# Performance work log

Hardware: AMD Instinct MI355X
Metric: run time of the kernel (lower is better)

Reference implementation:

```python
import math
import jax, jax.numpy as jnp
import numpy as np

NUM_EMBED = 2048
EMBED_FEATS = 64
IN_FEATS = 512
B, T = 16, 4096
COMMITMENT_COST = 0.25


def setup_inputs() -> dict:
    key = jax.random.key(0)
    k1, k2, k3, k4 = jax.random.split(key, 4)
    x = jax.random.normal(k1, (B, IN_FEATS, T), dtype=jnp.float32)
    proj_w = jax.random.normal(k2, (EMBED_FEATS, IN_FEATS), dtype=jnp.float32) / np.sqrt(IN_FEATS)
    proj_b = jax.random.normal(k3, (EMBED_FEATS,), dtype=jnp.float32) * 0.01
    embed = jax.random.normal(k4, (NUM_EMBED, EMBED_FEATS), dtype=jnp.float32)
    return {"x": x, "proj_w": proj_w, "proj_b": proj_b, "embed": embed}


def reference(x, proj_w, proj_b, embed):
    # 1x1 Conv1d projection, then transpose(1,-1): [B, Cin, T] -> [B, T, E]
    h = jnp.einsum('ec,bct->bte', proj_w, x) + proj_b  # [B, T, E]
    Bb, Tt, E = h.shape
    K = embed.shape[0]
    flat = h.reshape(-1, E)  # [N, E]
    # squared distances to codewords: [N, K]
    d2 = (jnp.sum(flat * flat, axis=1, keepdims=True)
          + jnp.sum(embed * embed, axis=1)
          - 2.0 * flat @ embed.T)
    q_idx = jnp.argmin(d2, axis=1)  # [N]
    z_q = embed[q_idx].reshape(Bb, Tt, E)  # one-hot @ embed == gather
    # commitment loss (codebook updated by EMA, so only commitment term)
    commitment = jnp.mean((jax.lax.stop_gradient(z_q) - h) ** 2)
    loss = COMMITMENT_COST * commitment
    # straight-through estimator
    z_q_st = h + jax.lax.stop_gradient(z_q - h)
    # code usage stats
    N = flat.shape[0]
    probs = jnp.zeros((K,), dtype=jnp.float32).at[q_idx].add(1.0) / N
    log_perplexity = -jnp.sum(probs * jnp.log(probs + 1e-10))
    kldiv_r = math.log(K) * (N / Bb) * jnp.ones((Bb, 1), dtype=jnp.float32)
    z_q_out = jnp.swapaxes(z_q_st, 1, 2)  # [B, E, T]
    return z_q_out, loss, kldiv_r, log_perplexity
```

## Files before the change

kernel.cpp:

```cpp
#include <hip/hip_runtime.h>
#include <math.h>

#define B_ 16
#define T_ 4096
#define C_ 512
#define E_ 64
#define K_ 2048
#define N_ (B_*T_)
#define ZQ_ELEMS 4194304

typedef __attribute__((ext_vector_type(8))) short short8;
typedef __attribute__((ext_vector_type(4))) short short4v;
typedef __attribute__((ext_vector_type(4))) float f32x4;

#define WS_EHI   0
#define WS_ELO   262144
#define WS_NHCC  524288
#define WS_WHI   532480
#define WS_WLO   598016
#define WS_HIST  663552
#define WS_LOSS  671744

struct HiLo { short hi, lo; };

__device__ __forceinline__ unsigned short rne16(float v) {
    unsigned u = __float_as_uint(v);
    return (unsigned short)((u + 0x7FFFu + ((u >> 16) & 1u)) >> 16);
}
__device__ __forceinline__ HiLo split_rne(float v) {
    HiLo r;
    unsigned hb = rne16(v);
    r.hi = (short)hb;
    float hf = __uint_as_float((unsigned)hb << 16);
    r.lo = (short)rne16(v - hf);
    return r;
}

__global__ void prep_kernel(const float* __restrict__ embed,
                            const float* __restrict__ W,
                            short* __restrict__ ehi, short* __restrict__ elo,
                            float* __restrict__ nhcc,
                            short* __restrict__ whi, short* __restrict__ wlo) {
    const int tid = threadIdx.x;
    if (blockIdx.x < 64) {
        const int row = blockIdx.x * 32 + (tid >> 3);
        const int g = tid & 7;
        const float* src = embed + (size_t)row * 64 + g * 8;
        short8 hv, lv;
        float s = 0.f;
#pragma unroll
        for (int j = 0; j < 8; ++j) {
            float v = src[j];
            s = fmaf(v, v, s);
            HiLo r = split_rne(v);
            hv[j] = r.hi; lv[j] = r.lo;
        }
        const int c128 = row >> 7, r = row & 127;
        const int kt = r >> 4, col = r & 15, ks = g >> 2, qe = g & 3;
        const int slot = (kt * 2 + ks) * 64 + qe * 16 + col;
        *(short8*)(ehi + c128 * 8192 + slot * 8) = hv;
        *(short8*)(elo + c128 * 8192 + slot * 8) = lv;
        s += __shfl_xor(s, 1, 64);
        s += __shfl_xor(s, 2, 64);
        s += __shfl_xor(s, 4, 64);
        if (g == 0) nhcc[row] = -0.5f * s;
    } else {
        int idx = ((blockIdx.x - 64) * 256 + tid) * 4;
        float4 v = *(const float4*)(W + idx);
        short4v h, l;
        HiLo a = split_rne(v.x); h[0] = a.hi; l[0] = a.lo;
        HiLo b = split_rne(v.y); h[1] = b.hi; l[1] = b.lo;
        HiLo c = split_rne(v.z); h[2] = c.hi; l[2] = c.lo;
        HiLo d = split_rne(v.w); h[3] = d.hi; l[3] = d.lo;
        *(short4v*)(whi + idx) = h;
        *(short4v*)(wlo + idx) = l;
    }
}

__global__ __launch_bounds__(256, 2) void projvq_kernel(
        const float* __restrict__ x,
        const short* __restrict__ whi, const short* __restrict__ wlo,
        const float* __restrict__ bias,
        const short* __restrict__ ehi, const short* __restrict__ elo,
        const float* __restrict__ nhcc,
        const float* __restrict__ embed, float* __restrict__ out,
        int* __restrict__ hist, float* __restrict__ lossacc) {
    __shared__ float smemf[8832];
    float* xs   = smemf;
    short* aimg = (short*)smemf;
    short* es   = (short*)smemf;
    float* ccs  = (float*)(smemf + 8192);
    float* tile = smemf;
    __shared__ int qs[128];

    const int tid = threadIdx.x;
    const int wave = tid >> 6, lane = tid & 63;
    const int row16 = lane & 15, quad = lane >> 4;
    const int b  = blockIdx.x >> 5;
    const int t0 = (blockIdx.x & 31) * 128;
    const float* xb = x + (size_t)b * C_ * T_ + t0;

    f32x4 cc0 = *(const f32x4*)(nhcc + tid * 8);
    f32x4 cc1 = *(const f32x4*)(nhcc + tid * 8 + 4);

    f32x4 acc[2][4];
#pragma unroll
    for (int i = 0; i < 2; ++i)
#pragma unroll
        for (int j = 0; j < 4; ++j) acc[i][j] = (f32x4){0.f, 0.f, 0.f, 0.f};

    const int xcc = tid >> 5;
    const int xtt = (tid & 31) * 4;
    float4 xpf[4];
#pragma unroll
    for (int j = 0; j < 4; ++j)
        xpf[j] = *(const float4*)(xb + (size_t)(xcc + j * 8) * T_ + xtt);

    for (int c0 = 0; c0 < C_; c0 += 32) {
#pragma unroll
        for (int j = 0; j < 4; ++j)
            *(float4*)(xs + (xcc + j * 8) * 136 + xtt) = xpf[j];
        __syncthreads();
        if (c0 < C_ - 32) {
#pragma unroll
            for (int j = 0; j < 4; ++j)
                xpf[j] = *(const float4*)(xb + (size_t)(c0 + 32 + xcc + j * 8) * T_ + xtt);
        }

        short8 bh[2], bl[2];
#pragma unroll
        for (int tt2 = 0; tt2 < 2; ++tt2) {
            int t = wave * 32 + tt2 * 16 + row16;
#pragma unroll
            for (int j = 0; j < 8; ++j) {
                float v = xs[(quad * 8 + j) * 136 + t];
                HiLo r = split_rne(v);
                bh[tt2][j] = r.hi; bl[tt2][j] = r.lo;
            }
        }
#pragma unroll
        for (int et = 0; et < 4; ++et) {
            size_t aoff = (size_t)(et * 16 + row16) * C_ + c0 + quad * 8;
            short8 ah = *(const short8*)(whi + aoff);
            short8 al = *(const short8*)(wlo + aoff);
#pragma unroll
            for (int tt2 = 0; tt2 < 2; ++tt2) {
                acc[tt2][et] = __builtin_amdgcn_mfma_f32_16x16x32_bf16(ah, bh[tt2], acc[tt2][et], 0, 0, 0);
                acc[tt2][et] = __builtin_amdgcn_mfma_f32_16x16x32_bf16(al, bh[tt2], acc[tt2][et], 0, 0, 0);
                acc[tt2][et] = __builtin_amdgcn_mfma_f32_16x16x32_bf16(ah, bl[tt2], acc[tt2][et], 0, 0, 0);
                acc[tt2][et] = __builtin_amdgcn_mfma_f32_16x16x32_bf16(al, bl[tt2], acc[tt2][et], 0, 0, 0);
            }
        }
        __syncthreads();
    }

    float hh = 0.f;
#pragma unroll
    for (int et = 0; et < 4; ++et) {
        float4 bv = *(const float4*)(bias + et * 16 + quad * 4);
#pragma unroll
        for (int tt2 = 0; tt2 < 2; ++tt2) {
            f32x4 a = acc[tt2][et];
            a[0] += bv.x; a[1] += bv.y; a[2] += bv.z; a[3] += bv.w;
            hh = fmaf(a[0], a[0], hh); hh = fmaf(a[1], a[1], hh);
            hh = fmaf(a[2], a[2], hh); hh = fmaf(a[3], a[3], hh);
            short4v hv, lv;
#pragma unroll
            for (int r = 0; r < 4; ++r) {
                HiLo sp = split_rne(a[r]);
                hv[r] = sp.hi; lv[r] = sp.lo;
            }
            const int ks = et >> 1;
            const int qe = (et & 1) * 2 + (quad >> 1);
            const int j0 = (quad & 1) * 4;
            const int sl = (((wave * 2 + tt2) * 2 + ks) * 64 + qe * 16 + row16) * 8 + j0;
            *(short4v*)(aimg + sl) = hv;
            *(short4v*)(aimg + 8192 + sl) = lv;
        }
    }
#pragma unroll
    for (int m = 1; m < 64; m <<= 1) hh += __shfl_xor(hh, m, 64);
    if (lane == 0) atomicAdd(lossacc, hh);
    __syncthreads();

    short8 a_hi[2][2], a_lo[2][2];
#pragma unroll
    for (int rt = 0; rt < 2; ++rt)
#pragma unroll
        for (int ks = 0; ks < 2; ++ks) {
            int sl = (((wave * 2 + rt) * 2 + ks) * 64 + lane) * 8;
            a_hi[rt][ks] = *(const short8*)(aimg + sl);
            a_lo[rt][ks] = *(const short8*)(aimg + 8192 + sl);
        }
    __syncthreads();

    short8 pf[8];
#pragma unroll
    for (int it = 0; it < 4; ++it) {
        pf[it]     = *(const short8*)(ehi + (it * 256 + tid) * 8);
        pf[4 + it] = *(const short8*)(elo + (it * 256 + tid) * 8);
    }

    float vmax[2][4];
    int   vidx[2][4];
#pragma unroll
    for (int rt = 0; rt < 2; ++rt)
#pragma unroll
        for (int rg = 0; rg < 4; ++rg) { vmax[rt][rg] = -3.4e38f; vidx[rt][rg] = 0; }

    for (int c = 0; c < 16; ++c) {
#pragma unroll
        for (int it = 0; it < 4; ++it) {
            *(short8*)(es + (it * 256 + tid) * 8)        = pf[it];
            *(short8*)(es + 8192 + (it * 256 + tid) * 8) = pf[4 + it];
        }
        if ((tid >> 4) == c) {
            int u = tid & 15;
            *(f32x4*)(ccs + u * 8)     = cc0;
            *(f32x4*)(ccs + u * 8 + 4) = cc1;
        }
        __syncthreads();
        if (c < 15) {
            const short* sh = ehi + (c + 1) * 8192;
            const short* sl2 = elo + (c + 1) * 8192;
#pragma unroll
            for (int it = 0; it < 4; ++it) {
                pf[it]     = *(const short8*)(sh + (it * 256 + tid) * 8);
                pf[4 + it] = *(const short8*)(sl2 + (it * 256 + tid) * 8);
            }
        }

#pragma unroll
        for (int kt = 0; kt < 8; ++kt) {
            const float ci = ccs[kt * 16 + row16];
            const short* pb = es + (kt * 2) * 512;
            short8 bh0 = *(const short8*)(pb + lane * 8);
            short8 bh1 = *(const short8*)(pb + 512 + lane * 8);
            short8 bl0 = *(const short8*)(pb + 8192 + lane * 8);
            short8 bl1 = *(const short8*)(pb + 8192 + 512 + lane * 8);
            const int kk = c * 128 + kt * 16 + row16;
#pragma unroll
            for (int rt = 0; rt < 2; ++rt) {
                f32x4 a2 = {0.f, 0.f, 0.f, 0.f};
                a2 = __builtin_amdgcn_mfma_f32_16x16x32_bf16(a_hi[rt][0], bh0, a2, 0, 0, 0);
                a2 = __builtin_amdgcn_mfma_f32_16x16x32_bf16(a_hi[rt][1], bh1, a2, 0, 0, 0);
                a2 = __builtin_amdgcn_mfma_f32_16x16x32_bf16(a_lo[rt][0], bh0, a2, 0, 0, 0);
                a2 = __builtin_amdgcn_mfma_f32_16x16x32_bf16(a_lo[rt][1], bh1, a2, 0, 0, 0);
                a2 = __builtin_amdgcn_mfma_f32_16x16x32_bf16(a_hi[rt][0], bl0, a2, 0, 0, 0);
                a2 = __builtin_amdgcn_mfma_f32_16x16x32_bf16(a_hi[rt][1], bl1, a2, 0, 0, 0);
#pragma unroll
                for (int rg = 0; rg < 4; ++rg) {
                    float v = a2[rg] + ci;
                    if (v > vmax[rt][rg]) { vmax[rt][rg] = v; vidx[rt][rg] = kk; }
                }
            }
        }
        __syncthreads();
    }

    float s = 0.f;
#pragma unroll
    for (int rt = 0; rt < 2; ++rt) {
#pragma unroll
        for (int rg = 0; rg < 4; ++rg) {
            float v = vmax[rt][rg];
            int ix = vidx[rt][rg];
#pragma unroll
            for (int m = 1; m < 16; m <<= 1) {
                float ov = __shfl_xor(v, m, 64);
                int   oi = __shfl_xor(ix, m, 64);
                if (ov > v || (ov == v && oi < ix)) { v = ov; ix = oi; }
            }
            if (row16 == 0) {
                qs[wave * 32 + rt * 16 + quad * 4 + rg] = ix;
                atomicAdd(&hist[ix], 1);
                s += v;
            }
        }
    }
    s += __shfl_xor(s, 16, 64);
    s += __shfl_xor(s, 32, 64);
    if (lane == 0) atomicAdd(lossacc, -2.f * s);
    __syncthreads();

    {
        const int r = tid >> 1, piece = tid & 1;
        const float* src = embed + (size_t)qs[r] * 64 + piece * 32;
#pragma unroll
        for (int j = 0; j < 8; ++j) {
            float4 v = *(const float4*)(src + j * 4);
            *(float4*)(tile + r * 69 + piece * 32 + j * 4) = v;
        }
    }
    __syncthreads();
    {
        const int tt = tid & 63;
        const int eo = tid >> 6;
        float* ob = out + ((size_t)b * 64) * T_ + t0;
#pragma unroll
        for (int j = 0; j < 16; ++j) {
            int e = j * 4 + eo;
            ob[(size_t)e * T_ + tt]      = tile[tt * 69 + e];
            ob[(size_t)e * T_ + 64 + tt] = tile[(tt + 64) * 69 + e];
        }
    }
}

__global__ void finalize_kernel(const int* __restrict__ hist,
                                const float* __restrict__ lossacc,
                                float* __restrict__ out) {
    __shared__ float red[4];
    const int tid = threadIdx.x;
    float s = 0.f;
    for (int k = tid; k < K_; k += 256) {
        float p = (float)hist[k] * (1.f / 65536.f);
        s -= p * logf(p + 1e-10f);
    }
#pragma unroll
    for (int m = 1; m < 64; m <<= 1) s += __shfl_xor(s, m, 64);
    if ((tid & 63) == 0) red[tid >> 6] = s;
    __syncthreads();
    if (tid == 0) {
        float lp = red[0] + red[1] + red[2] + red[3];
        out[ZQ_ELEMS] = 0.25f * lossacc[0] / (float)ZQ_ELEMS;
        out[ZQ_ELEMS + 17] = lp;
    }
    if (tid < 16) out[ZQ_ELEMS + 1 + tid] = logf(2048.f) * 4096.f;
}

extern "C" void kernel_launch(void* const* d_in, const int* in_sizes, int n_in,
                              void* d_out, int out_size, void* d_ws, size_t ws_size,
                              hipStream_t stream) {
    const float* x      = (const float*)d_in[0];
    const float* proj_w = (const float*)d_in[1];
    const float* proj_b = (const float*)d_in[2];
    const float* embed  = (const float*)d_in[3];
    float* out = (float*)d_out;
    char* ws = (char*)d_ws;

    short* e_hi = (short*)(ws + WS_EHI);
    short* e_lo = (short*)(ws + WS_ELO);
    float* nhcc = (float*)(ws + WS_NHCC);
    short* w_hi = (short*)(ws + WS_WHI);
    short* w_lo = (short*)(ws + WS_WLO);
    int*   hist = (int*)(ws + WS_HIST);
    float* lossac = (float*)(ws + WS_LOSS);

    (void)hipMemsetAsync(ws + WS_HIST, 0, K_ * sizeof(int) + sizeof(float), stream);

    prep_kernel<<<96, 256, 0, stream>>>(embed, proj_w, e_hi, e_lo, nhcc, w_hi, w_lo);
    projvq_kernel<<<N_ / 128, 256, 0, stream>>>(x, w_hi, w_lo, proj_b,
                                                e_hi, e_lo, nhcc, embed, out,
                                                hist, lossac);
    finalize_kernel<<<1, 256, 0, stream>>>(hist, lossac, out);
}
```

Before: 309.1 us.

## Double the block to 512 threads, split codebook halves, async global-to-LDS loads

The fused projection+VQ kernel moves to 512 threads per block. In the projection phase each wave now owns 16 time steps. In the VQ phase wave pairs split the 128-code chunk in half, and the two halves' argmax results are merged through shared memory. Global loads of x and codebook tiles go directly to LDS via global_load_lds into double buffers, replacing register prefetch and one barrier per chunk. This adds a larger LDS footprint (about 68 KB) that may cap occupancy, plus an extra cross-wave reduction step.

```diff
diff --git a/kernel.cpp b/kernel.cpp
--- a/kernel.cpp
+++ b/kernel.cpp
@@ -34,6 +34,12 @@
     float hf = __uint_as_float((unsigned)hb << 16);
     r.lo = (short)rne16(v - hf);
     return r;
+}
+
+typedef const __attribute__((address_space(1))) void* gas1_t;
+typedef __attribute__((address_space(3))) void* las3_t;
+__device__ __forceinline__ void gl16(const void* g, void* l) {
+    __builtin_amdgcn_global_load_lds((gas1_t)g, (las3_t)l, 16, 0, 0);
 }
 
 __global__ void prep_kernel(const float* __restrict__ embed,
@@ -77,7 +83,7 @@
     }
 }
 
-__global__ __launch_bounds__(256, 2) void projvq_kernel(
+__global__ __launch_bounds__(512, 4) void projvq_kernel(
         const float* __restrict__ x,
         const short* __restrict__ whi, const short* __restrict__ wlo,
         const float* __restrict__ bias,
@@ -85,13 +91,15 @@
         const float* __restrict__ nhcc,
         const float* __restrict__ embed, float* __restrict__ out,
         int* __restrict__ hist, float* __restrict__ lossacc) {
-    __shared__ float smemf[8832];
-    float* xs   = smemf;
-    short* aimg = (short*)smemf;
-    short* es   = (short*)smemf;
-    float* ccs  = (float*)(smemf + 8192);
-    float* tile = smemf;
-    __shared__ int qs[128];
+    __shared__ __align__(16) char smem[68096];
+    float* xsf  = (float*)smem;
+    short* es   = (short*)smem;
+    short* aimg = (short*)(smem + 32768);
+    float* ccs  = (float*)(smem + 65536);
+    int*   qsm  = (int*)(smem + 66560);
+    float* vtmp = (float*)(smem + 67072);
+    int*   itmp = (int*)(smem + 67584);
+    float* tile = (float*)smem;
 
     const int tid = threadIdx.x;
     const int wave = tid >> 6, lane = tid & 63;
@@ -100,106 +108,96 @@
     const int t0 = (blockIdx.x & 31) * 128;
     const float* xb = x + (size_t)b * C_ * T_ + t0;
 
-    f32x4 cc0 = *(const f32x4*)(nhcc + tid * 8);
-    f32x4 cc1 = *(const f32x4*)(nhcc + tid * 8 + 4);
-
-    f32x4 acc[2][4];
-#pragma unroll
-    for (int i = 0; i < 2; ++i)
-#pragma unroll
-        for (int j = 0; j < 4; ++j) acc[i][j] = (f32x4){0.f, 0.f, 0.f, 0.f};
-
-    const int xcc = tid >> 5;
-    const int xtt = (tid & 31) * 4;
-    float4 xpf[4];
-#pragma unroll
-    for (int j = 0; j < 4; ++j)
-        xpf[j] = *(const float4*)(xb + (size_t)(xcc + j * 8) * T_ + xtt);
-
-    for (int c0 = 0; c0 < C_; c0 += 32) {
-#pragma unroll
-        for (int j = 0; j < 4; ++j)
-            *(float4*)(xs + (xcc + j * 8) * 136 + xtt) = xpf[j];
-        __syncthreads();
-        if (c0 < C_ - 32) {
-#pragma unroll
-            for (int j = 0; j < 4; ++j)
-                xpf[j] = *(const float4*)(xb + (size_t)(c0 + 32 + xcc + j * 8) * T_ + xtt);
-        }
-
-        short8 bh[2], bl[2];
-#pragma unroll
-        for (int tt2 = 0; tt2 < 2; ++tt2) {
-            int t = wave * 32 + tt2 * 16 + row16;
-#pragma unroll
-            for (int j = 0; j < 8; ++j) {
-                float v = xs[(quad * 8 + j) * 136 + t];
-                HiLo r = split_rne(v);
-                bh[tt2][j] = r.hi; bl[tt2][j] = r.lo;
-            }
+    f32x4 cc = *(const f32x4*)(nhcc + tid * 4);
+
+    f32x4 acc[4];
+#pragma unroll
+    for (int et = 0; et < 4; ++et) acc[et] = (f32x4){0.f, 0.f, 0.f, 0.f};
+
+#pragma unroll
+    for (int j = 0; j < 2; ++j) {
+        int o = j * 512 + tid;
+        gl16(xb + (size_t)(o >> 5) * T_ + (o & 31) * 4, xsf + o * 4);
+    }
+    __syncthreads();
+
+    for (int it = 0; it < 16; ++it) {
+        const int c0 = it * 32;
+        const int p = it & 1;
+        if (it < 15) {
+#pragma unroll
+            for (int j = 0; j < 2; ++j) {
+                int o = j * 512 + tid;
+                gl16(xb + (size_t)(c0 + 32 + (o >> 5)) * T_ + (o & 31) * 4,
+                     xsf + (p ^ 1) * 4096 + o * 4);
+            }
+        }
+        const float* xsb = xsf + p * 4096;
+        short8 bh, bl;
+#pragma unroll
+        for (int j = 0; j < 8; ++j) {
+            float v = xsb[(quad * 8 + j) * 128 + wave * 16 + row16];
+            HiLo r = split_rne(v);
+            bh[j] = r.hi; bl[j] = r.lo;
         }
 #pragma unroll
         for (int et = 0; et < 4; ++et) {
             size_t aoff = (size_t)(et * 16 + row16) * C_ + c0 + quad * 8;
             short8 ah = *(const short8*)(whi + aoff);
             short8 al = *(const short8*)(wlo + aoff);
-#pragma unroll
-            for (int tt2 = 0; tt2 < 2; ++tt2) {
-                acc[tt2][et] = __builtin_amdgcn_mfma_f32_16x16x32_bf16(ah, bh[tt2], acc[tt2][et], 0, 0, 0);
-                acc[tt2][et] = __builtin_amdgcn_mfma_f32_16x16x32_bf16(al, bh[tt2], acc[tt2][et], 0, 0, 0);
-                acc[tt2][et] = __builtin_amdgcn_mfma_f32_16x16x32_bf16(ah, bl[tt2], acc[tt2][et], 0, 0, 0);
-                acc[tt2][et] = __builtin_amdgcn_mfma_f32_16x16x32_bf16(al, bl[tt2], acc[tt2][et], 0, 0, 0);
-            }
+            acc[et] = __builtin_amdgcn_mfma_f32_16x16x32_bf16(ah, bh, acc[et], 0, 0, 0);
+            acc[et] = __builtin_amdgcn_mfma_f32_16x16x32_bf16(al, bh, acc[et], 0, 0, 0);
+            acc[et] = __builtin_amdgcn_mfma_f32_16x16x32_bf16(ah, bl, acc[et], 0, 0, 0);
+            acc[et] = __builtin_amdgcn_mfma_f32_16x16x32_bf16(al, bl, acc[et], 0, 0, 0);
         }
         __syncthreads();
+    }
+
+#pragma unroll
+    for (int j = 0; j < 2; ++j) {
+        int o = (j * 512 + tid) * 8;
+        gl16(ehi + o, es + o);
+        gl16(elo + o, es + 8192 + o);
     }
 
     float hh = 0.f;
 #pragma unroll
     for (int et = 0; et < 4; ++et) {
         float4 bv = *(const float4*)(bias + et * 16 + quad * 4);
-#pragma unroll
-        for (int tt2 = 0; tt2 < 2; ++tt2) {
-            f32x4 a = acc[tt2][et];
-            a[0] += bv.x; a[1] += bv.y; a[2] += bv.z; a[3] += bv.w;
-            hh = fmaf(a[0], a[0], hh); hh = fmaf(a[1], a[1], hh);
-            hh = fmaf(a[2], a[2], hh); hh = fmaf(a[3], a[3], hh);
-            short4v hv, lv;
-#pragma unroll
-            for (int r = 0; r < 4; ++r) {
-                HiLo sp = split_rne(a[r]);
-                hv[r] = sp.hi; lv[r] = sp.lo;
-            }
-            const int ks = et >> 1;
-            const int qe = (et & 1) * 2 + (quad >> 1);
-            const int j0 = (quad & 1) * 4;
-            const int sl = (((wave * 2 + tt2) * 2 + ks) * 64 + qe * 16 + row16) * 8 + j0;
-            *(short4v*)(aimg + sl) = hv;
-            *(short4v*)(aimg + 8192 + sl) = lv;
-        }
+        f32x4 a = acc[et];
+        a[0] += bv.x; a[1] += bv.y; a[2] += bv.z; a[3] += bv.w;
+        hh = fmaf(a[0], a[0], hh); hh = fmaf(a[1], a[1], hh);
+        hh = fmaf(a[2], a[2], hh); hh = fmaf(a[3], a[3], hh);
+        short4v hv, lv;
+#pragma unroll
+        for (int r = 0; r < 4; ++r) {
+            HiLo sp = split_rne(a[r]);
+            hv[r] = sp.hi; lv[r] = sp.lo;
+        }
+        const int ks = et >> 1;
+        const int qe = (et & 1) * 2 + (quad >> 1);
+        const int j0 = (quad & 1) * 4;
+        const int sl = ((wave * 2 + ks) * 64 + qe * 16 + row16) * 8 + j0;
+        *(short4v*)(aimg + sl) = hv;
+        *(short4v*)(aimg + 8192 + sl) = lv;
     }
 #pragma unroll
     for (int m = 1; m < 64; m <<= 1) hh += __shfl_xor(hh, m, 64);
     if (lane == 0) atomicAdd(lossacc, hh);
     __syncthreads();
 
+    const int pair = wave & 3, kh = wave >> 2;
     short8 a_hi[2][2], a_lo[2][2];
 #pragma unroll
     for (int rt = 0; rt < 2; ++rt)
 #pragma unroll
         for (int ks = 0; ks < 2; ++ks) {
-            int sl = (((wave * 2 + rt) * 2 + ks) * 64 + lane) * 8;
+            int sl = (((2 * pair + rt) * 2 + ks) * 64 + lane) * 8;
             a_hi[rt][ks] = *(const short8*)(aimg + sl);
             a_lo[rt][ks] = *(const short8*)(aimg + 8192 + sl);
         }
-    __syncthreads();
-
-    short8 pf[8];
-#pragma unroll
-    for (int it = 0; it < 4; ++it) {
-        pf[it]     = *(const short8*)(ehi + (it * 256 + tid) * 8);
-        pf[4 + it] = *(const short8*)(elo + (it * 256 + tid) * 8);
-    }
+    if ((tid >> 5) == 0) *(f32x4*)(ccs + (tid & 31) * 4) = cc;
+    __syncthreads();
 
     float vmax[2][4];
     int   vidx[2][4];
@@ -209,31 +207,26 @@
         for (int rg = 0; rg < 4; ++rg) { vmax[rt][rg] = -3.4e38f; vidx[rt][rg] = 0; }
 
     for (int c = 0; c < 16; ++c) {
-#pragma unroll
-        for (int it = 0; it < 4; ++it) {
-            *(short8*)(es + (it * 256 + tid) * 8)        = pf[it];
-            *(short8*)(es + 8192 + (it * 256 + tid) * 8) = pf[4 + it];
-        }
-        if ((tid >> 4) == c) {
-            int u = tid & 15;
-            *(f32x4*)(ccs + u * 8)     = cc0;
-            *(f32x4*)(ccs + u * 8 + 4) = cc1;
-        }
-        __syncthreads();
         if (c < 15) {
-            const short* sh = ehi + (c + 1) * 8192;
+            const short* sh  = ehi + (c + 1) * 8192;
             const short* sl2 = elo + (c + 1) * 8192;
-#pragma unroll
-            for (int it = 0; it < 4; ++it) {
-                pf[it]     = *(const short8*)(sh + (it * 256 + tid) * 8);
-                pf[4 + it] = *(const short8*)(sl2 + (it * 256 + tid) * 8);
-            }
-        }
-
-#pragma unroll
-        for (int kt = 0; kt < 8; ++kt) {
-            const float ci = ccs[kt * 16 + row16];
-            const short* pb = es + (kt * 2) * 512;
+            short* dst = es + ((c + 1) & 1) * 16384;
+#pragma unroll
+            for (int j = 0; j < 2; ++j) {
+                int o = (j * 512 + tid) * 8;
+                gl16(sh + o, dst + o);
+                gl16(sl2 + o, dst + 8192 + o);
+            }
+            if ((tid >> 5) == c + 1)
+                *(f32x4*)(ccs + ((c + 1) & 1) * 128 + (tid & 31) * 4) = cc;
+        }
+        const short* eb = es + (c & 1) * 16384;
+        const float* cb = ccs + (c & 1) * 128;
+#pragma unroll
+        for (int k4 = 0; k4 < 4; ++k4) {
+            const int kt = kh * 4 + k4;
+            const float ci = cb[kt * 16 + row16];
+            const short* pb = eb + kt * 1024;
             short8 bh0 = *(const short8*)(pb + lane * 8);
             short8 bh1 = *(const short8*)(pb + 512 + lane * 8);
             short8 bl0 = *(const short8*)(pb + 8192 + lane * 8);
@@ -241,7 +234,7 @@
             const int kk = c * 128 + kt * 16 + row16;
 #pragma unroll
             for (int rt = 0; rt < 2; ++rt) {
-                f32x4 a2 = {0.f, 0.f, 0.f, 0.f};
+                f32x4 a2 = (f32x4){0.f, 0.f, 0.f, 0.f};
                 a2 = __builtin_amdgcn_mfma_f32_16x16x32_bf16(a_hi[rt][0], bh0, a2, 0, 0, 0);
                 a2 = __builtin_amdgcn_mfma_f32_16x16x32_bf16(a_hi[rt][1], bh1, a2, 0, 0, 0);
                 a2 = __builtin_amdgcn_mfma_f32_16x16x32_bf16(a_lo[rt][0], bh0, a2, 0, 0, 0);
@@ -260,7 +253,7 @@
 
     float s = 0.f;
 #pragma unroll
-    for (int rt = 0; rt < 2; ++rt) {
+    for (int rt = 0; rt < 2; ++rt)
 #pragma unroll
         for (int rg = 0; rg < 4; ++rg) {
             float v = vmax[rt][rg];
@@ -271,26 +264,49 @@
                 int   oi = __shfl_xor(ix, m, 64);
                 if (ov > v || (ov == v && oi < ix)) { v = ov; ix = oi; }
             }
-            if (row16 == 0) {
-                qs[wave * 32 + rt * 16 + quad * 4 + rg] = ix;
-                atomicAdd(&hist[ix], 1);
-                s += v;
-            }
-        }
-    }
-    s += __shfl_xor(s, 16, 64);
-    s += __shfl_xor(s, 32, 64);
-    if (lane == 0) atomicAdd(lossacc, -2.f * s);
+            vmax[rt][rg] = v; vidx[rt][rg] = ix;
+        }
+    if (kh == 1 && row16 == 0) {
+#pragma unroll
+        for (int rt = 0; rt < 2; ++rt)
+#pragma unroll
+            for (int rg = 0; rg < 4; ++rg) {
+                const int row = (2 * pair + rt) * 16 + quad * 4 + rg;
+                vtmp[row] = vmax[rt][rg];
+                itmp[row] = vidx[rt][rg];
+            }
+    }
+    __syncthreads();
+    if (kh == 0) {
+        if (row16 == 0) {
+#pragma unroll
+            for (int rt = 0; rt < 2; ++rt)
+#pragma unroll
+                for (int rg = 0; rg < 4; ++rg) {
+                    const int row = (2 * pair + rt) * 16 + quad * 4 + rg;
+                    float v = vmax[rt][rg];
+                    int ix = vidx[rt][rg];
+                    const float ov = vtmp[row];
+                    const int   oi = itmp[row];
+                    if (ov > v || (ov == v && oi < ix)) { v = ov; ix = oi; }
+                    qsm[row] = ix;
+                    atomicAdd(&hist[ix], 1);
+                    s += v;
+                }
+        }
+        s += __shfl_xor(s, 16, 64);
+        s += __shfl_xor(s, 32, 64);
+        if (lane == 0) atomicAdd(lossacc, -2.f * s);
+    }
     __syncthreads();
 
     {
-        const int r = tid >> 1, piece = tid & 1;
-        const float* src = embed + (size_t)qs[r] * 64 + piece * 32;
-#pragma unroll
-        for (int j = 0; j < 8; ++j) {
-            float4 v = *(const float4*)(src + j * 4);
-            *(float4*)(tile + r * 69 + piece * 32 + j * 4) = v;
-        }
+        const int r = tid >> 2, piece = tid & 3;
+        const float* src = embed + (size_t)qsm[r] * 64 + piece * 16;
+        float* dst = tile + r * 69 + piece * 16;
+#pragma unroll
+        for (int j = 0; j < 4; ++j)
+            *(float4*)(dst + j * 4) = *(const float4*)(src + j * 4);
     }
     __syncthreads();
     {
@@ -298,8 +314,8 @@
         const int eo = tid >> 6;
         float* ob = out + ((size_t)b * 64) * T_ + t0;
 #pragma unroll
-        for (int j = 0; j < 16; ++j) {
-            int e = j * 4 + eo;
+        for (int j = 0; j < 8; ++j) {
+            const int e = j * 8 + eo;
             ob[(size_t)e * T_ + tt]      = tile[tt * 69 + e];
             ob[(size_t)e * T_ + 64 + tt] = tile[(tt + 64) * 69 + e];
         }
@@ -349,7 +365,7 @@
     (void)hipMemsetAsync(ws + WS_HIST, 0, K_ * sizeof(int) + sizeof(float), stream);
 
     prep_kernel<<<96, 256, 0, stream>>>(embed, proj_w, e_hi, e_lo, nhcc, w_hi, w_lo);
-    projvq_kernel<<<N_ / 128, 256, 0, stream>>>(x, w_hi, w_lo, proj_b,
+    projvq_kernel<<<N_ / 128, 512, 0, stream>>>(x, w_hi, w_lo, proj_b,
                                                 e_hi, e_lo, nhcc, embed, out,
                                                 hist, lossac);
     finalize_kernel<<<1, 256, 0, stream>>>(hist, lossac, out);
```

Result: no change. 309.8 us (+0.2%).

## Split projection over channels and codebook search over waves with 64-token tiles

Applied to the files above, without the earlier changes.

Each block now handles 64 tokens instead of 128, doubling the block count. In the projection each wave reduces a quarter of the input channels, and the partial sums are combined through shared memory. In the search each wave scans a quarter of the codebook straight from global/L2 with register double-buffering, replacing the LDS staging and its per-chunk barriers, and per-wave argmins are merged in shared memory. The histogram memset is folded into the prep kernel. The cost is a larger shared-memory footprint, extra reduction barriers, and serial work confined to a single wave.

```diff
diff --git a/kernel.cpp b/kernel.cpp
--- a/kernel.cpp
+++ b/kernel.cpp
@@ -40,8 +40,12 @@
                             const float* __restrict__ W,
                             short* __restrict__ ehi, short* __restrict__ elo,
                             float* __restrict__ nhcc,
-                            short* __restrict__ whi, short* __restrict__ wlo) {
+                            short* __restrict__ whi, short* __restrict__ wlo,
+                            int* __restrict__ hist) {
     const int tid = threadIdx.x;
+    if (blockIdx.x == 0) {
+        for (int i = tid; i < K_ + 1; i += 256) hist[i] = 0;
+    }
     if (blockIdx.x < 64) {
         const int row = blockIdx.x * 32 + (tid >> 3);
         const int g = tid & 7;
@@ -77,7 +81,39 @@
     }
 }
 
-__global__ __launch_bounds__(256, 2) void projvq_kernel(
+#define VQ_STEP(H0, H1, L0, L1, SS)                                            \
+    {                                                                          \
+        const int kk = ((SS) >> 1) * 128 + (kh * 2 + ((SS) & 1)) * 16 + row16; \
+        const float ci = nhcc[kk];                                             \
+        _Pragma("unroll")                                                      \
+        for (int rt = 0; rt < 4; ++rt) {                                       \
+            f32x4 a2 = (f32x4){0.f, 0.f, 0.f, 0.f};                            \
+            a2 = __builtin_amdgcn_mfma_f32_16x16x32_bf16(a_hi[rt][0], H0, a2, 0, 0, 0); \
+            a2 = __builtin_amdgcn_mfma_f32_16x16x32_bf16(a_hi[rt][1], H1, a2, 0, 0, 0); \
+            a2 = __builtin_amdgcn_mfma_f32_16x16x32_bf16(a_lo[rt][0], H0, a2, 0, 0, 0); \
+            a2 = __builtin_amdgcn_mfma_f32_16x16x32_bf16(a_lo[rt][1], H1, a2, 0, 0, 0); \
+            a2 = __builtin_amdgcn_mfma_f32_16x16x32_bf16(a_hi[rt][0], L0, a2, 0, 0, 0); \
+            a2 = __builtin_amdgcn_mfma_f32_16x16x32_bf16(a_hi[rt][1], L1, a2, 0, 0, 0); \
+            _Pragma("unroll")                                                  \
+            for (int rg = 0; rg < 4; ++rg) {                                   \
+                float v = a2[rg] + ci;                                         \
+                if (v > vmax[rt][rg]) { vmax[rt][rg] = v; vidx[rt][rg] = kk; } \
+            }                                                                  \
+        }                                                                      \
+    }
+
+#define VQ_LOAD(H0, H1, L0, L1, SS)                                            \
+    {                                                                          \
+        const int c2 = (SS) >> 1, kt2 = kh * 2 + ((SS) & 1);                   \
+        const short* pb = ehi + c2 * 8192 + kt2 * 1024;                        \
+        const short* pl = elo + c2 * 8192 + kt2 * 1024;                        \
+        H0 = *(const short8*)(pb + lane * 8);                                  \
+        H1 = *(const short8*)(pb + 512 + lane * 8);                            \
+        L0 = *(const short8*)(pl + lane * 8);                                  \
+        L1 = *(const short8*)(pl + 512 + lane * 8);                            \
+    }
+
+__global__ __launch_bounds__(256, 2) void fused_kernel(
         const float* __restrict__ x,
         const short* __restrict__ whi, const short* __restrict__ wlo,
         const float* __restrict__ bias,
@@ -85,182 +121,181 @@
         const float* __restrict__ nhcc,
         const float* __restrict__ embed, float* __restrict__ out,
         int* __restrict__ hist, float* __restrict__ lossacc) {
-    __shared__ float smemf[8832];
-    float* xs   = smemf;
-    short* aimg = (short*)smemf;
-    short* es   = (short*)smemf;
-    float* ccs  = (float*)(smemf + 8192);
-    float* tile = smemf;
-    __shared__ int qs[128];
+    __shared__ __align__(16) char smem[36608];
+    float* xw   = (float*)smem;
+    float* M1   = (float*)smem;
+    float* M2   = (float*)(smem + 17408);
+    short* H    = (short*)smem;
+    float* tile = (float*)smem;
+    int*   qsm  = (int*)(smem + 34816);
+    float* vtmp = (float*)(smem + 35072);
+    int*   itmp = (int*)(smem + 35840);
 
     const int tid = threadIdx.x;
     const int wave = tid >> 6, lane = tid & 63;
     const int row16 = lane & 15, quad = lane >> 4;
-    const int b  = blockIdx.x >> 5;
-    const int t0 = (blockIdx.x & 31) * 128;
-    const float* xb = x + (size_t)b * C_ * T_ + t0;
-
-    f32x4 cc0 = *(const f32x4*)(nhcc + tid * 8);
-    f32x4 cc1 = *(const f32x4*)(nhcc + tid * 8 + 4);
-
-    f32x4 acc[2][4];
-#pragma unroll
-    for (int i = 0; i < 2; ++i)
-#pragma unroll
-        for (int j = 0; j < 4; ++j) acc[i][j] = (f32x4){0.f, 0.f, 0.f, 0.f};
-
-    const int xcc = tid >> 5;
-    const int xtt = (tid & 31) * 4;
-    float4 xpf[4];
-#pragma unroll
-    for (int j = 0; j < 4; ++j)
-        xpf[j] = *(const float4*)(xb + (size_t)(xcc + j * 8) * T_ + xtt);
-
-    for (int c0 = 0; c0 < C_; c0 += 32) {
-#pragma unroll
-        for (int j = 0; j < 4; ++j)
-            *(float4*)(xs + (xcc + j * 8) * 136 + xtt) = xpf[j];
-        __syncthreads();
-        if (c0 < C_ - 32) {
-#pragma unroll
-            for (int j = 0; j < 4; ++j)
-                xpf[j] = *(const float4*)(xb + (size_t)(c0 + 32 + xcc + j * 8) * T_ + xtt);
-        }
-
-        short8 bh[2], bl[2];
-#pragma unroll
-        for (int tt2 = 0; tt2 < 2; ++tt2) {
-            int t = wave * 32 + tt2 * 16 + row16;
-#pragma unroll
-            for (int j = 0; j < 8; ++j) {
-                float v = xs[(quad * 8 + j) * 136 + t];
-                HiLo r = split_rne(v);
-                bh[tt2][j] = r.hi; bl[tt2][j] = r.lo;
-            }
-        }
-#pragma unroll
-        for (int et = 0; et < 4; ++et) {
-            size_t aoff = (size_t)(et * 16 + row16) * C_ + c0 + quad * 8;
-            short8 ah = *(const short8*)(whi + aoff);
-            short8 al = *(const short8*)(wlo + aoff);
-#pragma unroll
-            for (int tt2 = 0; tt2 < 2; ++tt2) {
-                acc[tt2][et] = __builtin_amdgcn_mfma_f32_16x16x32_bf16(ah, bh[tt2], acc[tt2][et], 0, 0, 0);
-                acc[tt2][et] = __builtin_amdgcn_mfma_f32_16x16x32_bf16(al, bh[tt2], acc[tt2][et], 0, 0, 0);
-                acc[tt2][et] = __builtin_amdgcn_mfma_f32_16x16x32_bf16(ah, bl[tt2], acc[tt2][et], 0, 0, 0);
-                acc[tt2][et] = __builtin_amdgcn_mfma_f32_16x16x32_bf16(al, bl[tt2], acc[tt2][et], 0, 0, 0);
-            }
-        }
-        __syncthreads();
-    }
-
-    float hh = 0.f;
-#pragma unroll
-    for (int et = 0; et < 4; ++et) {
-        float4 bv = *(const float4*)(bias + et * 16 + quad * 4);
-#pragma unroll
-        for (int tt2 = 0; tt2 < 2; ++tt2) {
-            f32x4 a = acc[tt2][et];
-            a[0] += bv.x; a[1] += bv.y; a[2] += bv.z; a[3] += bv.w;
-            hh = fmaf(a[0], a[0], hh); hh = fmaf(a[1], a[1], hh);
-            hh = fmaf(a[2], a[2], hh); hh = fmaf(a[3], a[3], hh);
-            short4v hv, lv;
-#pragma unroll
-            for (int r = 0; r < 4; ++r) {
-                HiLo sp = split_rne(a[r]);
-                hv[r] = sp.hi; lv[r] = sp.lo;
-            }
-            const int ks = et >> 1;
-            const int qe = (et & 1) * 2 + (quad >> 1);
-            const int j0 = (quad & 1) * 4;
-            const int sl = (((wave * 2 + tt2) * 2 + ks) * 64 + qe * 16 + row16) * 8 + j0;
-            *(short4v*)(aimg + sl) = hv;
-            *(short4v*)(aimg + 8192 + sl) = lv;
-        }
-    }
-#pragma unroll
-    for (int m = 1; m < 64; m <<= 1) hh += __shfl_xor(hh, m, 64);
-    if (lane == 0) atomicAdd(lossacc, hh);
-    __syncthreads();
-
-    short8 a_hi[2][2], a_lo[2][2];
-#pragma unroll
-    for (int rt = 0; rt < 2; ++rt)
-#pragma unroll
-        for (int ks = 0; ks < 2; ++ks) {
-            int sl = (((wave * 2 + rt) * 2 + ks) * 64 + lane) * 8;
-            a_hi[rt][ks] = *(const short8*)(aimg + sl);
-            a_lo[rt][ks] = *(const short8*)(aimg + 8192 + sl);
-        }
-    __syncthreads();
-
-    short8 pf[8];
-#pragma unroll
+    const int blk = blockIdx.x;
+    const int b  = blk >> 6;
+    const int t0 = (blk & 63) * 64;
+    const float* xr = x + (size_t)b * C_ * T_ + t0;
+    float* wl = xw + wave * (32 * 66);
+
+    const int c_row = lane >> 4;
+    const int c_t4  = (lane & 15) * 4;
+    const int cbase = wave * 128;
+
+    f32x4 acc[4][4];
+#pragma unroll
+    for (int rt = 0; rt < 4; ++rt)
+#pragma unroll
+        for (int et = 0; et < 4; ++et) acc[rt][et] = (f32x4){0.f, 0.f, 0.f, 0.f};
+
+    float4 xn[8];
+#pragma unroll
+    for (int q = 0; q < 8; ++q)
+        xn[q] = *(const float4*)(xr + (size_t)(cbase + q * 4 + c_row) * T_ + c_t4);
+
     for (int it = 0; it < 4; ++it) {
-        pf[it]     = *(const short8*)(ehi + (it * 256 + tid) * 8);
-        pf[4 + it] = *(const short8*)(elo + (it * 256 + tid) * 8);
-    }
-
-    float vmax[2][4];
-    int   vidx[2][4];
-#pragma unroll
-    for (int rt = 0; rt < 2; ++rt)
-#pragma unroll
-        for (int rg = 0; rg < 4; ++rg) { vmax[rt][rg] = -3.4e38f; vidx[rt][rg] = 0; }
-
-    for (int c = 0; c < 16; ++c) {
-#pragma unroll
-        for (int it = 0; it < 4; ++it) {
-            *(short8*)(es + (it * 256 + tid) * 8)        = pf[it];
-            *(short8*)(es + 8192 + (it * 256 + tid) * 8) = pf[4 + it];
-        }
-        if ((tid >> 4) == c) {
-            int u = tid & 15;
-            *(f32x4*)(ccs + u * 8)     = cc0;
-            *(f32x4*)(ccs + u * 8 + 4) = cc1;
-        }
-        __syncthreads();
-        if (c < 15) {
-            const short* sh = ehi + (c + 1) * 8192;
-            const short* sl2 = elo + (c + 1) * 8192;
-#pragma unroll
-            for (int it = 0; it < 4; ++it) {
-                pf[it]     = *(const short8*)(sh + (it * 256 + tid) * 8);
-                pf[4 + it] = *(const short8*)(sl2 + (it * 256 + tid) * 8);
-            }
-        }
-
-#pragma unroll
-        for (int kt = 0; kt < 8; ++kt) {
-            const float ci = ccs[kt * 16 + row16];
-            const short* pb = es + (kt * 2) * 512;
-            short8 bh0 = *(const short8*)(pb + lane * 8);
-            short8 bh1 = *(const short8*)(pb + 512 + lane * 8);
-            short8 bl0 = *(const short8*)(pb + 8192 + lane * 8);
-            short8 bl1 = *(const short8*)(pb + 8192 + 512 + lane * 8);
-            const int kk = c * 128 + kt * 16 + row16;
-#pragma unroll
-            for (int rt = 0; rt < 2; ++rt) {
-                f32x4 a2 = {0.f, 0.f, 0.f, 0.f};
-                a2 = __builtin_amdgcn_mfma_f32_16x16x32_bf16(a_hi[rt][0], bh0, a2, 0, 0, 0);
-                a2 = __builtin_amdgcn_mfma_f32_16x16x32_bf16(a_hi[rt][1], bh1, a2, 0, 0, 0);
-                a2 = __builtin_amdgcn_mfma_f32_16x16x32_bf16(a_lo[rt][0], bh0, a2, 0, 0, 0);
-                a2 = __builtin_amdgcn_mfma_f32_16x16x32_bf16(a_lo[rt][1], bh1, a2, 0, 0, 0);
-                a2 = __builtin_amdgcn_mfma_f32_16x16x32_bf16(a_hi[rt][0], bl0, a2, 0, 0, 0);
-                a2 = __builtin_amdgcn_mfma_f32_16x16x32_bf16(a_hi[rt][1], bl1, a2, 0, 0, 0);
-#pragma unroll
-                for (int rg = 0; rg < 4; ++rg) {
-                    float v = a2[rg] + ci;
-                    if (v > vmax[rt][rg]) { vmax[rt][rg] = v; vidx[rt][rg] = kk; }
+        const int c0 = cbase + it * 32;
+#pragma unroll
+        for (int q = 0; q < 8; ++q) {
+            float* d = wl + (q * 4 + c_row) * 66 + c_t4;
+            *(float2*)(d)     = make_float2(xn[q].x, xn[q].y);
+            *(float2*)(d + 2) = make_float2(xn[q].z, xn[q].w);
+        }
+        if (it < 3) {
+#pragma unroll
+            for (int q = 0; q < 8; ++q)
+                xn[q] = *(const float4*)(xr + (size_t)(c0 + 32 + q * 4 + c_row) * T_ + c_t4);
+        }
+#pragma unroll
+        for (int rp = 0; rp < 2; ++rp) {
+            short8 bh[2], bl[2];
+#pragma unroll
+            for (int rr = 0; rr < 2; ++rr) {
+                const int rt = rp * 2 + rr;
+#pragma unroll
+                for (int j = 0; j < 8; ++j) {
+                    float v = wl[(quad * 8 + j) * 66 + rt * 16 + row16];
+                    HiLo r = split_rne(v);
+                    bh[rr][j] = r.hi; bl[rr][j] = r.lo;
                 }
             }
-        }
-        __syncthreads();
-    }
-
-    float s = 0.f;
-#pragma unroll
-    for (int rt = 0; rt < 2; ++rt) {
+#pragma unroll
+            for (int et = 0; et < 4; ++et) {
+                size_t aoff = (size_t)(et * 16 + row16) * C_ + c0 + quad * 8;
+                short8 ah = *(const short8*)(whi + aoff);
+                short8 al = *(const short8*)(wlo + aoff);
+#pragma unroll
+                for (int rr = 0; rr < 2; ++rr) {
+                    const int rt = rp * 2 + rr;
+                    acc[rt][et] = __builtin_amdgcn_mfma_f32_16x16x32_bf16(ah, bh[rr], acc[rt][et], 0, 0, 0);
+                    acc[rt][et] = __builtin_amdgcn_mfma_f32_16x16x32_bf16(al, bh[rr], acc[rt][et], 0, 0, 0);
+                    acc[rt][et] = __builtin_amdgcn_mfma_f32_16x16x32_bf16(ah, bl[rr], acc[rt][et], 0, 0, 0);
+                    acc[rt][et] = __builtin_amdgcn_mfma_f32_16x16x32_bf16(al, bl[rr], acc[rt][et], 0, 0, 0);
+                }
+            }
+        }
+    }
+
+    __syncthreads();
+    if (wave == 1 || wave == 3) {
+        float* Mx = (wave == 1) ? M1 : M2;
+#pragma unroll
+        for (int rt = 0; rt < 4; ++rt)
+#pragma unroll
+            for (int et = 0; et < 4; ++et)
+#pragma unroll
+                for (int r = 0; r < 4; ++r)
+                    Mx[(et * 16 + quad * 4 + r) * 68 + rt * 16 + row16] = acc[rt][et][r];
+    }
+    __syncthreads();
+    if (wave == 0 || wave == 2) {
+        float* Mx = (wave == 0) ? M1 : M2;
+#pragma unroll
+        for (int rt = 0; rt < 4; ++rt)
+#pragma unroll
+            for (int et = 0; et < 4; ++et)
+#pragma unroll
+                for (int r = 0; r < 4; ++r)
+                    acc[rt][et][r] += Mx[(et * 16 + quad * 4 + r) * 68 + rt * 16 + row16];
+    }
+    __syncthreads();
+    if (wave == 2) {
+#pragma unroll
+        for (int rt = 0; rt < 4; ++rt)
+#pragma unroll
+            for (int et = 0; et < 4; ++et)
+#pragma unroll
+                for (int r = 0; r < 4; ++r)
+                    M1[(et * 16 + quad * 4 + r) * 68 + rt * 16 + row16] = acc[rt][et][r];
+    }
+    __syncthreads();
+    if (wave == 0) {
+        float hh = 0.f;
+#pragma unroll
+        for (int rt = 0; rt < 4; ++rt) {
+#pragma unroll
+            for (int et = 0; et < 4; ++et) {
+                float4 bv = *(const float4*)(bias + et * 16 + quad * 4);
+                f32x4 a = acc[rt][et];
+#pragma unroll
+                for (int r = 0; r < 4; ++r)
+                    a[r] += M1[(et * 16 + quad * 4 + r) * 68 + rt * 16 + row16];
+                a[0] += bv.x; a[1] += bv.y; a[2] += bv.z; a[3] += bv.w;
+                hh = fmaf(a[0], a[0], hh); hh = fmaf(a[1], a[1], hh);
+                hh = fmaf(a[2], a[2], hh); hh = fmaf(a[3], a[3], hh);
+                short4v hv, lv;
+#pragma unroll
+                for (int r = 0; r < 4; ++r) {
+                    HiLo sp = split_rne(a[r]);
+                    hv[r] = sp.hi; lv[r] = sp.lo;
+                }
+                const int ks = et >> 1;
+                const int qe = (et & 1) * 2 + (quad >> 1);
+                const int j0 = (quad & 1) * 4;
+                const int sl = ((rt * 2 + ks) * 64 + qe * 16 + row16) * 8 + j0;
+                *(short4v*)(H + sl) = hv;
+                *(short4v*)(H + 8192 + sl) = lv;
+            }
+        }
+#pragma unroll
+        for (int m = 1; m < 64; m <<= 1) hh += __shfl_xor(hh, m, 64);
+        if (lane == 0) atomicAdd(lossacc, hh);
+    }
+    __syncthreads();
+
+    const int kh = wave;
+    short8 a_hi[4][2], a_lo[4][2];
+#pragma unroll
+    for (int rt = 0; rt < 4; ++rt)
+#pragma unroll
+        for (int ks = 0; ks < 2; ++ks) {
+            const int sl = ((rt * 2 + ks) * 64 + lane) * 8;
+            a_hi[rt][ks] = *(const short8*)(H + sl);
+            a_lo[rt][ks] = *(const short8*)(H + 8192 + sl);
+        }
+
+    float vmax[4][4];
+    int   vidx[4][4];
+#pragma unroll
+    for (int rt = 0; rt < 4; ++rt)
+#pragma unroll
+        for (int rg = 0; rg < 4; ++rg) { vmax[rt][rg] = -3.4e38f; vidx[rt][rg] = 0; }
+
+    short8 pAh0, pAh1, pAl0, pAl1;
+    short8 pBh0, pBh1, pBl0, pBl1;
+    VQ_LOAD(pAh0, pAh1, pAl0, pAl1, 0);
+    for (int s = 0; s < 32; s += 2) {
+        VQ_LOAD(pBh0, pBh1, pBl0, pBl1, s + 1);
+        VQ_STEP(pAh0, pAh1, pAl0, pAl1, s);
+        if (s + 2 < 32) VQ_LOAD(pAh0, pAh1, pAl0, pAl1, s + 2);
+        VQ_STEP(pBh0, pBh1, pBl0, pBl1, s + 1);
+    }
+
+    float s_loss = 0.f;
+#pragma unroll
+    for (int rt = 0; rt < 4; ++rt)
 #pragma unroll
         for (int rg = 0; rg < 4; ++rg) {
             float v = vmax[rt][rg];
@@ -271,26 +306,52 @@
                 int   oi = __shfl_xor(ix, m, 64);
                 if (ov > v || (ov == v && oi < ix)) { v = ov; ix = oi; }
             }
-            if (row16 == 0) {
-                qs[wave * 32 + rt * 16 + quad * 4 + rg] = ix;
-                atomicAdd(&hist[ix], 1);
-                s += v;
+            vmax[rt][rg] = v; vidx[rt][rg] = ix;
+        }
+    if (kh >= 1 && row16 == 0) {
+#pragma unroll
+        for (int rt = 0; rt < 4; ++rt)
+#pragma unroll
+            for (int rg = 0; rg < 4; ++rg) {
+                const int row = rt * 16 + quad * 4 + rg;
+                vtmp[(kh - 1) * 64 + row] = vmax[rt][rg];
+                itmp[(kh - 1) * 64 + row] = vidx[rt][rg];
             }
-        }
-    }
-    s += __shfl_xor(s, 16, 64);
-    s += __shfl_xor(s, 32, 64);
-    if (lane == 0) atomicAdd(lossacc, -2.f * s);
+    }
+    __syncthreads();
+    if (kh == 0) {
+        if (row16 == 0) {
+#pragma unroll
+            for (int rt = 0; rt < 4; ++rt)
+#pragma unroll
+                for (int rg = 0; rg < 4; ++rg) {
+                    const int row = rt * 16 + quad * 4 + rg;
+                    float v = vmax[rt][rg];
+                    int ix = vidx[rt][rg];
+#pragma unroll
+                    for (int p = 0; p < 3; ++p) {
+                        const float ov = vtmp[p * 64 + row];
+                        const int   oi = itmp[p * 64 + row];
+                        if (ov > v || (ov == v && oi < ix)) { v = ov; ix = oi; }
+                    }
+                    qsm[row] = ix;
+                    atomicAdd(&hist[ix], 1);
+                    s_loss += v;
+                }
+        }
+        s_loss += __shfl_xor(s_loss, 16, 64);
+        s_loss += __shfl_xor(s_loss, 32, 64);
+        if (lane == 0) atomicAdd(lossacc, -2.f * s_loss);
+    }
     __syncthreads();
 
     {
-        const int r = tid >> 1, piece = tid & 1;
-        const float* src = embed + (size_t)qs[r] * 64 + piece * 32;
-#pragma unroll
-        for (int j = 0; j < 8; ++j) {
-            float4 v = *(const float4*)(src + j * 4);
-            *(float4*)(tile + r * 69 + piece * 32 + j * 4) = v;
-        }
+        const int r = tid >> 2, piece = tid & 3;
+        const float* src = embed + (size_t)qsm[r] * 64 + piece * 16;
+        float* dst = tile + r * 69 + piece * 16;
+#pragma unroll
+        for (int j = 0; j < 4; ++j)
+            *(float4*)(dst + j * 4) = *(const float4*)(src + j * 4);
     }
     __syncthreads();
     {
@@ -299,9 +360,8 @@
         float* ob = out + ((size_t)b * 64) * T_ + t0;
 #pragma unroll
         for (int j = 0; j < 16; ++j) {
-            int e = j * 4 + eo;
-            ob[(size_t)e * T_ + tt]      = tile[tt * 69 + e];
-            ob[(size_t)e * T_ + 64 + tt] = tile[(tt + 64) * 69 + e];
+            const int e = j * 4 + eo;
+            ob[(size_t)e * T_ + tt] = tile[tt * 69 + e];
         }
     }
 }
@@ -346,11 +406,10 @@
     int*   hist = (int*)(ws + WS_HIST);
     float* lossac = (float*)(ws + WS_LOSS);
 
-    (void)hipMemsetAsync(ws + WS_HIST, 0, K_ * sizeof(int) + sizeof(float), stream);
-
-    prep_kernel<<<96, 256, 0, stream>>>(embed, proj_w, e_hi, e_lo, nhcc, w_hi, w_lo);
-    projvq_kernel<<<N_ / 128, 256, 0, stream>>>(x, w_hi, w_lo, proj_b,
-                                                e_hi, e_lo, nhcc, embed, out,
-                                                hist, lossac);
+    prep_kernel<<<96, 256, 0, stream>>>(embed, proj_w, e_hi, e_lo, nhcc,
+                                        w_hi, w_lo, hist);
+    fused_kernel<<<1024, 256, 0, stream>>>(x, w_hi, w_lo, proj_b,
+                                           e_hi, e_lo, nhcc, embed, out,
+                                           hist, lossac);
     finalize_kernel<<<1, 256, 0, stream>>>(hist, lossac, out);
 }
```

Measured after the change: 271.3 us. 1.14x faster.
